# Kernel optimization log

Measured on AMD Instinct MI355X. Metric: run time of the kernel, lower is better.

The kernel has to match this reference:

```python
import jax, jax.numpy as jnp
import numpy as np

B, L, DIM = 2, 2048, 1024
H, DH, W = 16, 64, 256  # heads, head_dim, window_size
ROPE_BASE = 10000.0


def _rope(x):
    # x: [b, l, h, d] -> rotate consecutive pairs (torch view_as_complex semantics)
    l, d = x.shape[1], x.shape[3]
    freqs = 1.0 / (ROPE_BASE ** (jnp.arange(0, d, 2, dtype=jnp.float32) / d))  # [d/2]
    ang = jnp.arange(l, dtype=jnp.float32)[:, None] * freqs[None, :]           # [l, d/2]
    cos = jnp.cos(ang)[None, :, None, :].astype(x.dtype)
    sin = jnp.sin(ang)[None, :, None, :].astype(x.dtype)
    xe, xo = x[..., 0::2], x[..., 1::2]
    ye = xe * cos - xo * sin
    yo = xe * sin + xo * cos
    return jnp.stack([ye, yo], axis=-1).reshape(x.shape)


def setup_inputs() -> dict:
    key = jax.random.key(0)
    ks = jax.random.split(key, 7)
    sh = (B, L, DIM)
    return {
        "q": jax.random.normal(ks[0], sh, jnp.float32),
        "k": jax.random.normal(ks[1], sh, jnp.float32),
        "v": jax.random.normal(ks[2], sh, jnp.float32),
        "wq": jax.random.normal(ks[3], (H * DH, DIM), jnp.float32) * 0.02,
        "wk": jax.random.normal(ks[4], (H * DH, DIM), jnp.float32) * 0.02,
        "wv": jax.random.normal(ks[5], (H * DH, DIM), jnp.float32) * 0.02,
        "wo": jax.random.normal(ks[6], (DIM, H * DH), jnp.float32) * 0.02,
    }


def reference(q, k, v, wq, wk, wv, wo):
    b, l, _ = q.shape
    qh = (q @ wq.T).reshape(b, l, H, DH)
    kh = (k @ wk.T).reshape(b, l, H, DH)
    vh = (v @ wv.T).reshape(b, l, H, DH).transpose(0, 2, 1, 3)  # [b,h,l,d]
    qh = _rope(qh).transpose(0, 2, 1, 3)                        # [b,h,l,d]
    kh = _rope(kh).transpose(0, 2, 1, 3)
    scores = jnp.einsum('bhqd,bhkd->bhqk', qh, kh) * (DH ** -0.5)
    i = jnp.arange(l)[:, None]
    j = jnp.arange(l)[None, :]
    window_mask = (j <= i) & (j >= i - W)  # keys in [i-W, i], matches the loop
    scores = jnp.where(window_mask, scores, -1e30)
    probs = jax.nn.softmax(scores, axis=-1)
    out = jnp.einsum('bhqk,bhkd->bhqd', probs, vh)
    out = out.transpose(0, 2, 1, 3).reshape(b, l, H * DH)
    return out @ wo.T
```

## Files before the change

kernel.cpp:

```cpp
#include <hip/hip_runtime.h>
#include <stdint.h>

#define B_    2
#define L_    2048
#define DIM_  1024
#define H_    16
#define DH_   64
#define WWIN  256

typedef __attribute__((ext_vector_type(4))) float f32x4;
typedef __attribute__((ext_vector_type(8))) short bf16x8;

__device__ __forceinline__ unsigned short f2bf(float x) {
  union { float f; unsigned u; } c; c.f = x;
  unsigned r = c.u + 0x7fffu + ((c.u >> 16) & 1u);
  return (unsigned short)(r >> 16);
}

struct CastArgs {
  const float* src[7];
  unsigned short* dst[7];
};
__global__ __launch_bounds__(256) void cast_bf16_kernel(CastArgs a) {
  int bid = blockIdx.x;
  int arr, base;
  if (bid < 12288) {
    arr = bid >> 12;
    base = (bid & 4095) << 10;
  } else {
    int t = bid - 12288;
    arr = 3 + (t >> 10);
    base = (t & 1023) << 10;
  }
  int i = base + (int)threadIdx.x * 4;
  float4 v = *(const float4*)(a.src[arr] + i);
  ushort4 o;
  o.x = f2bf(v.x); o.y = f2bf(v.y); o.z = f2bf(v.z); o.w = f2bf(v.w);
  *(ushort4*)(a.dst[arr] + i) = o;
}

#define BM 128

__device__ __forceinline__ void gld_lds16(const void* g, void* l) {
  __builtin_amdgcn_global_load_lds(
      (const __attribute__((address_space(1))) void*)g,
      (__attribute__((address_space(3))) void*)l, 16, 0, 0);
}

__device__ __forceinline__ void gemm_core_128x128(
    const unsigned short* __restrict__ A, const unsigned short* __restrict__ Bt,
    unsigned short* As, unsigned short* Bs, f32x4 (&acc)[4][4],
    int m0, int n0) {
  const int tid = threadIdx.x;
  const int wave = tid >> 6, lane = tid & 63;
  const int quad = lane >> 4, l16 = lane & 15;
  const int wm = wave >> 1, wn = wave & 1;
  const int srow = tid >> 3, sc = tid & 7;

  auto stage = [&](int k0, int buf) {
    unsigned short* Ad = As + buf * 8192;
    unsigned short* Bd = Bs + buf * 8192;
    #pragma unroll
    for (int rd = 0; rd < 4; ++rd) {
      int row = rd * 32 + srow;
      int cs = sc ^ (row & 7);
      gld_lds16(A + (size_t)(m0 + row) * 1024 + k0 + cs * 8, Ad + row * 64 + sc * 8);
    }
    #pragma unroll
    for (int rd = 0; rd < 4; ++rd) {
      int row = rd * 32 + srow;
      int cs = sc ^ (row & 7);
      gld_lds16(Bt + (size_t)(n0 + row) * 1024 + k0 + cs * 8, Bd + row * 64 + sc * 8);
    }
  };

  stage(0, 0);
  for (int k = 0; k < 16; ++k) {
    const int cur = k & 1;
    __syncthreads();
    if (k < 15) stage((k + 1) * 64, cur ^ 1);
    const unsigned short* Ac = As + cur * 8192;
    const unsigned short* Bc = Bs + cur * 8192;
    #pragma unroll
    for (int ks = 0; ks < 2; ++ks) {
      bf16x8 af[4], bfr[4];
      #pragma unroll
      for (int i = 0; i < 4; ++i) {
        int row = wm * 64 + i * 16 + l16;
        int ch = (ks * 4 + quad) ^ (row & 7);
        af[i] = *(const bf16x8*)(Ac + row * 64 + ch * 8);
      }
      #pragma unroll
      for (int j = 0; j < 4; ++j) {
        int row = wn * 64 + j * 16 + l16;
        int ch = (ks * 4 + quad) ^ (row & 7);
        bfr[j] = *(const bf16x8*)(Bc + row * 64 + ch * 8);
      }
      #pragma unroll
      for (int i = 0; i < 4; ++i)
        #pragma unroll
        for (int j = 0; j < 4; ++j)
          acc[i][j] = __builtin_amdgcn_mfma_f32_16x16x32_bf16(af[i], bfr[j], acc[i][j], 0, 0, 0);
    }
  }
}

struct ProjArgs {
  const unsigned short* A[3];
  const unsigned short* Bt[3];
  unsigned short* C[3];
};
__global__ __launch_bounds__(256) void gemm_proj_kernel(ProjArgs pa) {
  __shared__ unsigned short SH[32768];
  unsigned short* As = SH;
  unsigned short* Bs = SH + 16384;

  const int bflat = blockIdx.x;
  const int xcd = bflat & 7, s = bflat >> 3;
  const int nblk = s & 7;
  const int mz = xcd * 12 + (s >> 3);
  const int z = mz >> 5;
  const int mblk = mz & 31;
  const int m0 = mblk * BM, n0 = nblk * 128;

  f32x4 acc[4][4] = {};
  gemm_core_128x128(pa.A[z], pa.Bt[z], As, Bs, acc, m0, n0);

  const int tid = threadIdx.x;
  const int lane = tid & 63, wave = tid >> 6;
  const int quad = lane >> 4, l16 = lane & 15;
  const int wm = wave >> 1, wn = wave & 1;
  const int h = nblk * 2 + wn;

  if (z < 2) {
    float frev[4];
    #pragma unroll
    for (int j = 0; j < 4; ++j) {
      int d = j * 16 + l16;
      frev[j] = exp2f(-(float)(d >> 1) * 0.41524101186092029f) * 0.15915494309189535f;
    }
    unsigned short* C = pa.C[z];
    const bool even = (l16 & 1) == 0;
    #pragma unroll
    for (int i = 0; i < 4; ++i)
      #pragma unroll
      for (int r = 0; r < 4; ++r) {
        int m = m0 + wm * 64 + i * 16 + quad * 4 + r;
        int b = m >> 11, l = m & (L_ - 1);
        float lf = (float)l;
        #pragma unroll
        for (int j = 0; j < 4; ++j) {
          int d = j * 16 + l16;
          float v = acc[i][j][r];
          float p = __shfl_xor(v, 1);
          float a = lf * frev[j];
          float t = a - floorf(a);
          float sn = __builtin_amdgcn_sinf(t);
          float cs = __builtin_amdgcn_cosf(t);
          float o = even ? (v * cs - p * sn) : (p * sn + v * cs);
          C[(((size_t)b * H_ + h) * L_ + l) * DH_ + d] = f2bf(o);
        }
      }
  } else {
    __syncthreads();
    char* T = (char*)SH + wave * 8192;
    #pragma unroll
    for (int i = 0; i < 4; ++i)
      #pragma unroll
      for (int j = 0; j < 4; ++j) {
        int d = j * 16 + l16;
        int mb = i * 32 + quad * 8;
        int ch = mb >> 4, sub = mb & 15;
        uint2 pk;
        pk.x = (unsigned)f2bf(acc[i][j][0]) | ((unsigned)f2bf(acc[i][j][1]) << 16);
        pk.y = (unsigned)f2bf(acc[i][j][2]) | ((unsigned)f2bf(acc[i][j][3]) << 16);
        *(uint2*)(T + d * 128 + ((ch ^ (d & 7)) << 4) + sub) = pk;
      }
    asm volatile("s_waitcnt lgkmcnt(0)" ::: "memory");
    int b = m0 >> 11;
    int lbase = (m0 & (L_ - 1)) + wm * 64;
    unsigned short* C = pa.C[2];
    #pragma unroll
    for (int t = 0; t < 8; ++t) {
      int d = t * 8 + (lane >> 3);
      int ch = lane & 7;
      uint4 o = *(uint4*)(T + d * 128 + ((ch ^ (d & 7)) << 4));
      *(uint4*)(C + (((size_t)b * H_ + h) * DH_ + d) * L_ + lbase + ch * 8) = o;
    }
  }
}

__global__ __launch_bounds__(256) void gemm_out_kernel(
    const unsigned short* __restrict__ A, const unsigned short* __restrict__ Bt,
    float* __restrict__ C) {
  __shared__ unsigned short SH[32768];
  unsigned short* As = SH;
  unsigned short* Bs = SH + 16384;

  const int bflat = blockIdx.x;
  const int xcd = bflat & 7, s = bflat >> 3;
  const int nblk = s & 7;
  const int mblk = xcd * 4 + (s >> 3);
  const int m0 = mblk * BM, n0 = nblk * 128;

  f32x4 acc[4][4] = {};
  gemm_core_128x128(A, Bt, As, Bs, acc, m0, n0);

  const int lane = threadIdx.x & 63, wave = threadIdx.x >> 6;
  const int quad = lane >> 4, l16 = lane & 15;
  const int wm = wave >> 1, wn = wave & 1;
  #pragma unroll
  for (int i = 0; i < 4; ++i)
    #pragma unroll
    for (int j = 0; j < 4; ++j)
      #pragma unroll
      for (int r = 0; r < 4; ++r) {
        int m = m0 + wm * 64 + i * 16 + quad * 4 + r;
        int n = n0 + wn * 64 + j * 16 + l16;
        C[(size_t)m * DIM_ + n] = acc[i][j][r];
      }
}

#define NCH 20
__global__ __launch_bounds__(256) void attn_kernel(
    const unsigned short* __restrict__ Qh,
    const unsigned short* __restrict__ Kh,
    const unsigned short* __restrict__ Vt,
    unsigned short* __restrict__ O) {
  __shared__ unsigned short KVs[64 * 168];
  __shared__ unsigned short Ps[4][16 * 172];
  const int tid = threadIdx.x;
  const int wave = tid >> 6, lane = tid & 63;
  const int quad = lane >> 4, l16 = lane & 15;

  const int bflat = blockIdx.x;
  const int xcd = bflat & 7, s = bflat >> 3;
  const int qt = s >> 2;
  const int bh = xcd * 4 + (s & 3);

  const int q0 = qt * 64;
  const int kwin0 = q0 - WWIN;
  const int qb = q0 + wave * 16;
  const bool edge = (kwin0 < 0);

  bf16x8 qf0, qf1;
  {
    const unsigned short* qrow = Qh + ((size_t)bh * L_ + qb + l16) * DH_;
    qf0 = *(const bf16x8*)(qrow + quad * 8);
    qf1 = *(const bf16x8*)(qrow + 32 + quad * 8);
  }

  f32x4 S[NCH] = {};

  const int srow = tid >> 3, sc = tid & 7;
  #pragma unroll
  for (int half = 0; half < 2; ++half) {
    __syncthreads();
    #pragma unroll
    for (int rep = 0; rep < 5; ++rep) {
      int row = rep * 32 + srow;
      int key = kwin0 + half * 160 + row;
      key = key < 0 ? 0 : key;
      int cs = sc ^ (row & 7);
      gld_lds16(Kh + ((size_t)bh * L_ + key) * DH_ + cs * 8,
                (unsigned short*)KVs + row * 64 + sc * 8);
    }
    __syncthreads();
    #pragma unroll
    for (int cc = 0; cc < 10; ++cc) {
      const int c = half * 10 + cc;
      if (c < wave || c > wave + 16) continue;
      int row = cc * 16 + l16;
      const unsigned short* kr = (const unsigned short*)KVs + row * 64;
      bf16x8 kf0 = *(const bf16x8*)(kr + ((quad) ^ (row & 7)) * 8);
      bf16x8 kf1 = *(const bf16x8*)(kr + ((4 + quad) ^ (row & 7)) * 8);
      S[c] = __builtin_amdgcn_mfma_f32_16x16x32_bf16(qf0, kf0, S[c], 0, 0, 0);
      S[c] = __builtin_amdgcn_mfma_f32_16x16x32_bf16(qf1, kf1, S[c], 0, 0, 0);
    }
  }

  float inv_l[4];
  #pragma unroll
  for (int r = 0; r < 4; ++r) {
    const int i = qb + quad * 4 + r;
    float mx = -1e30f;
    #pragma unroll
    for (int c = 0; c < NCH; ++c) {
      if (c < wave || c > wave + 16) continue;
      float v = S[c][r];
      if (edge || c == wave || c == wave + 16) {
        int key = kwin0 + c * 16 + l16;
        bool valid = (key >= 0) && (key <= i) && (key >= i - WWIN);
        v = valid ? v : -1e30f;
        S[c][r] = v;
      }
      mx = fmaxf(mx, v);
    }
    mx = fmaxf(mx, __shfl_xor(mx, 1));
    mx = fmaxf(mx, __shfl_xor(mx, 2));
    mx = fmaxf(mx, __shfl_xor(mx, 4));
    mx = fmaxf(mx, __shfl_xor(mx, 8));
    float sum = 0.f;
    #pragma unroll
    for (int c = 0; c < NCH; ++c) {
      if (c < wave || c > wave + 16) continue;
      float e = __builtin_amdgcn_exp2f((S[c][r] - mx) * 0.18033688011112042f);
      S[c][r] = e;
      sum += e;
    }
    sum += __shfl_xor(sum, 1);
    sum += __shfl_xor(sum, 2);
    sum += __shfl_xor(sum, 4);
    sum += __shfl_xor(sum, 8);
    inv_l[r] = 1.0f / sum;
  }

  f32x4 Oacc[4] = {};
  unsigned short* pw = &Ps[wave][0];
  #pragma unroll
  for (int half = 0; half < 2; ++half) {
    const int glo = (half == 0) ? (wave >> 1) : 0;
    const int ghi = (half == 0) ? 4 : ((wave + 6) >> 1);
    __syncthreads();
    for (int rep = 0; rep < 5; ++rep) {
      int ci = rep * 256 + tid;
      int row = ci / 20, c = ci % 20;
      int key0 = kwin0 + half * 160 + c * 8;
      uint4 val = {0, 0, 0, 0};
      if (key0 >= 0)
        val = *(const uint4*)(Vt + ((size_t)bh * DH_ + row) * L_ + key0);
      *(uint4*)(&KVs[row * 168 + c * 8]) = val;
    }
    #pragma unroll
    for (int cc = 0; cc < 10; ++cc) {
      if ((cc >> 1) < glo || (cc >> 1) > ghi) continue;
      #pragma unroll
      for (int r = 0; r < 4; ++r) {
        float p = S[half * 10 + cc][r] * inv_l[r];
        pw[(quad * 4 + r) * 172 + cc * 16 + l16] = f2bf(p);
      }
    }
    __syncthreads();
    #pragma unroll
    for (int s5 = 0; s5 < 5; ++s5) {
      if (s5 < glo || s5 > ghi) continue;
      bf16x8 pf = *(const bf16x8*)(pw + l16 * 172 + s5 * 32 + quad * 8);
      int lk = s5 * 32 + quad * 8;
      #pragma unroll
      for (int t = 0; t < 4; ++t) {
        bf16x8 vf = *(const bf16x8*)(&KVs[(t * 16 + l16) * 168 + lk]);
        Oacc[t] = __builtin_amdgcn_mfma_f32_16x16x32_bf16(pf, vf, Oacc[t], 0, 0, 0);
      }
    }
  }

  int b = bh >> 4, h = bh & 15;
  #pragma unroll
  for (int t = 0; t < 4; ++t)
    #pragma unroll
    for (int r = 0; r < 4; ++r) {
      int l = qb + quad * 4 + r;
      int col = h * DH_ + t * 16 + l16;
      O[((size_t)b * L_ + l) * (H_ * DH_) + col] = f2bf(Oacc[t][r]);
    }
}

extern "C" void kernel_launch(void* const* d_in, const int* in_sizes, int n_in,
                              void* d_out, int out_size, void* d_ws, size_t ws_size,
                              hipStream_t stream) {
  const float* q  = (const float*)d_in[0];
  const float* k  = (const float*)d_in[1];
  const float* v  = (const float*)d_in[2];
  const float* wq = (const float*)d_in[3];
  const float* wk = (const float*)d_in[4];
  const float* wv = (const float*)d_in[5];
  const float* wo = (const float*)d_in[6];

  const size_t SA = (size_t)B_ * L_ * DIM_;
  const size_t SW = (size_t)DIM_ * DIM_;
  unsigned short* w   = (unsigned short*)d_ws;
  unsigned short* qb  = w; w += SA;
  unsigned short* kb  = w; w += SA;
  unsigned short* vb  = w; w += SA;
  unsigned short* wqb = w; w += SW;
  unsigned short* wkb = w; w += SW;
  unsigned short* wvb = w; w += SW;
  unsigned short* wob = w; w += SW;
  unsigned short* qh  = w; w += SA;
  unsigned short* kh  = w; w += SA;
  unsigned short* vt  = w; w += SA;
  unsigned short* Ob  = w; w += SA;

  CastArgs ca;
  ca.src[0] = q;  ca.dst[0] = qb;
  ca.src[1] = k;  ca.dst[1] = kb;
  ca.src[2] = v;  ca.dst[2] = vb;
  ca.src[3] = wq; ca.dst[3] = wqb;
  ca.src[4] = wk; ca.dst[4] = wkb;
  ca.src[5] = wv; ca.dst[5] = wvb;
  ca.src[6] = wo; ca.dst[6] = wob;
  cast_bf16_kernel<<<dim3(16384), 256, 0, stream>>>(ca);

  ProjArgs pa;
  pa.A[0] = qb; pa.Bt[0] = wqb; pa.C[0] = qh;
  pa.A[1] = kb; pa.Bt[1] = wkb; pa.C[1] = kh;
  pa.A[2] = vb; pa.Bt[2] = wvb; pa.C[2] = vt;
  gemm_proj_kernel<<<dim3(768), 256, 0, stream>>>(pa);

  attn_kernel<<<dim3(32 * 32), 256, 0, stream>>>(qh, kh, vt, Ob);
  gemm_out_kernel<<<dim3(256), 256, 0, stream>>>(Ob, wob, (float*)d_out);
}
```

Baseline: 196.4 us.

## Load K/V fragments per wave from global, dropping LDS staging and barriers

The attention kernel no longer stages K and V tiles into shared memory for the whole block. Each wave now reads its own 17-chunk key window straight from global memory into MFMA operands, and only its probability tile goes through LDS, so every __syncthreads is gone. Each wave also covers exactly its window instead of a shared 20-chunk range with per-wave skipping. In exchange, the four waves read overlapping K/V rows redundantly through the cache hierarchy, and the per-lane global fragment loads are less coalesced than the cooperative LDS fills.

After: 207.6 us. +5.7%, slower.

```diff
diff --git a/kernel.cpp b/kernel.cpp
--- a/kernel.cpp
+++ b/kernel.cpp
@@ -221,14 +221,13 @@
       }
 }
 
-#define NCH 20
+#define PSTR 292
 __global__ __launch_bounds__(256) void attn_kernel(
     const unsigned short* __restrict__ Qh,
     const unsigned short* __restrict__ Kh,
     const unsigned short* __restrict__ Vt,
     unsigned short* __restrict__ O) {
-  __shared__ unsigned short KVs[64 * 168];
-  __shared__ unsigned short Ps[4][16 * 172];
+  __shared__ unsigned short Ps[4][16 * PSTR];
   const int tid = threadIdx.x;
   const int wave = tid >> 6, lane = tid & 63;
   const int quad = lane >> 4, l16 = lane & 15;
@@ -238,10 +237,14 @@
   const int qt = s >> 2;
   const int bh = xcd * 4 + (s & 3);
 
-  const int q0 = qt * 64;
-  const int kwin0 = q0 - WWIN;
-  const int qb = q0 + wave * 16;
-  const bool edge = (kwin0 < 0);
+  const int qb = qt * 64 + wave * 16;
+  const int kw0 = qb - WWIN;
+  const bool edge = (kw0 < 0);
+
+  unsigned short* pw = &Ps[wave][0];
+  #pragma unroll
+  for (int r = 0; r < 4; ++r)
+    pw[(quad * 4 + r) * PSTR + 272 + l16] = 0;
 
   bf16x8 qf0, qf1;
   {
@@ -250,46 +253,30 @@
     qf1 = *(const bf16x8*)(qrow + 32 + quad * 8);
   }
 
-  f32x4 S[NCH] = {};
-
-  const int srow = tid >> 3, sc = tid & 7;
-  #pragma unroll
-  for (int half = 0; half < 2; ++half) {
-    __syncthreads();
-    #pragma unroll
-    for (int rep = 0; rep < 5; ++rep) {
-      int row = rep * 32 + srow;
-      int key = kwin0 + half * 160 + row;
-      key = key < 0 ? 0 : key;
-      int cs = sc ^ (row & 7);
-      gld_lds16(Kh + ((size_t)bh * L_ + key) * DH_ + cs * 8,
-                (unsigned short*)KVs + row * 64 + sc * 8);
-    }
-    __syncthreads();
-    #pragma unroll
-    for (int cc = 0; cc < 10; ++cc) {
-      const int c = half * 10 + cc;
-      if (c < wave || c > wave + 16) continue;
-      int row = cc * 16 + l16;
-      const unsigned short* kr = (const unsigned short*)KVs + row * 64;
-      bf16x8 kf0 = *(const bf16x8*)(kr + ((quad) ^ (row & 7)) * 8);
-      bf16x8 kf1 = *(const bf16x8*)(kr + ((4 + quad) ^ (row & 7)) * 8);
-      S[c] = __builtin_amdgcn_mfma_f32_16x16x32_bf16(qf0, kf0, S[c], 0, 0, 0);
-      S[c] = __builtin_amdgcn_mfma_f32_16x16x32_bf16(qf1, kf1, S[c], 0, 0, 0);
-    }
+  f32x4 S[17] = {};
+  const unsigned short* kbase = Kh + (size_t)bh * L_ * DH_;
+  #pragma unroll
+  for (int c = 0; c < 17; ++c) {
+    int key = kw0 + c * 16 + l16;
+    key = key < 0 ? 0 : key;
+    const unsigned short* kr = kbase + (size_t)key * DH_ + quad * 8;
+    bf16x8 kf0 = *(const bf16x8*)(kr);
+    bf16x8 kf1 = *(const bf16x8*)(kr + 32);
+    S[c] = __builtin_amdgcn_mfma_f32_16x16x32_bf16(qf0, kf0, S[c], 0, 0, 0);
+    S[c] = __builtin_amdgcn_mfma_f32_16x16x32_bf16(qf1, kf1, S[c], 0, 0, 0);
   }
 
   float inv_l[4];
   #pragma unroll
   for (int r = 0; r < 4; ++r) {
-    const int i = qb + quad * 4 + r;
+    const int qr = quad * 4 + r;
+    const int i = qb + qr;
     float mx = -1e30f;
     #pragma unroll
-    for (int c = 0; c < NCH; ++c) {
-      if (c < wave || c > wave + 16) continue;
+    for (int c = 0; c < 17; ++c) {
       float v = S[c][r];
-      if (edge || c == wave || c == wave + 16) {
-        int key = kwin0 + c * 16 + l16;
+      if (c == 0 || c == 16 || edge) {
+        int key = kw0 + c * 16 + l16;
         bool valid = (key >= 0) && (key <= i) && (key >= i - WWIN);
         v = valid ? v : -1e30f;
         S[c][r] = v;
@@ -302,8 +289,7 @@
     mx = fmaxf(mx, __shfl_xor(mx, 8));
     float sum = 0.f;
     #pragma unroll
-    for (int c = 0; c < NCH; ++c) {
-      if (c < wave || c > wave + 16) continue;
+    for (int c = 0; c < 17; ++c) {
       float e = __builtin_amdgcn_exp2f((S[c][r] - mx) * 0.18033688011112042f);
       S[c][r] = e;
       sum += e;
@@ -315,42 +301,25 @@
     inv_l[r] = 1.0f / sum;
   }
 
+  #pragma unroll
+  for (int c = 0; c < 17; ++c)
+    #pragma unroll
+    for (int r = 0; r < 4; ++r)
+      pw[(quad * 4 + r) * PSTR + c * 16 + l16] = f2bf(S[c][r] * inv_l[r]);
+  asm volatile("s_waitcnt lgkmcnt(0)" ::: "memory");
+
   f32x4 Oacc[4] = {};
-  unsigned short* pw = &Ps[wave][0];
-  #pragma unroll
-  for (int half = 0; half < 2; ++half) {
-    const int glo = (half == 0) ? (wave >> 1) : 0;
-    const int ghi = (half == 0) ? 4 : ((wave + 6) >> 1);
-    __syncthreads();
-    for (int rep = 0; rep < 5; ++rep) {
-      int ci = rep * 256 + tid;
-      int row = ci / 20, c = ci % 20;
-      int key0 = kwin0 + half * 160 + c * 8;
-      uint4 val = {0, 0, 0, 0};
-      if (key0 >= 0)
-        val = *(const uint4*)(Vt + ((size_t)bh * DH_ + row) * L_ + key0);
-      *(uint4*)(&KVs[row * 168 + c * 8]) = val;
-    }
-    #pragma unroll
-    for (int cc = 0; cc < 10; ++cc) {
-      if ((cc >> 1) < glo || (cc >> 1) > ghi) continue;
-      #pragma unroll
-      for (int r = 0; r < 4; ++r) {
-        float p = S[half * 10 + cc][r] * inv_l[r];
-        pw[(quad * 4 + r) * 172 + cc * 16 + l16] = f2bf(p);
-      }
-    }
-    __syncthreads();
-    #pragma unroll
-    for (int s5 = 0; s5 < 5; ++s5) {
-      if (s5 < glo || s5 > ghi) continue;
-      bf16x8 pf = *(const bf16x8*)(pw + l16 * 172 + s5 * 32 + quad * 8);
-      int lk = s5 * 32 + quad * 8;
-      #pragma unroll
-      for (int t = 0; t < 4; ++t) {
-        bf16x8 vf = *(const bf16x8*)(&KVs[(t * 16 + l16) * 168 + lk]);
-        Oacc[t] = __builtin_amdgcn_mfma_f32_16x16x32_bf16(pf, vf, Oacc[t], 0, 0, 0);
-      }
+  const unsigned short* vbase = Vt + (size_t)bh * DH_ * L_;
+  #pragma unroll
+  for (int g = 0; g < 9; ++g) {
+    bf16x8 pf = *(const bf16x8*)(pw + l16 * PSTR + g * 32 + quad * 8);
+    int vk = kw0 + g * 32 + quad * 8;
+    vk = vk < 0 ? 0 : vk;
+    vk = vk > (L_ - 8) ? (L_ - 8) : vk;
+    #pragma unroll
+    for (int t = 0; t < 4; ++t) {
+      bf16x8 vf = *(const bf16x8*)(vbase + (size_t)(t * 16 + l16) * L_ + vk);
+      Oacc[t] = __builtin_amdgcn_mfma_f32_16x16x32_bf16(pf, vf, Oacc[t], 0, 0, 0);
     }
   }
 
```
